# Kernel tuning notes

Measured on AMD Instinct MI355X. Metric: run time of the kernel, lower is better.

Reference implementation:

```python
import jax, jax.numpy as jnp
import numpy as np

N_NODES = 50000
N_EDGES = 800000
IN_DIM = 128
HEADS = 8
HEAD_DIM = 16


def setup_inputs() -> dict:
    key = jax.random.key(0)
    ks = jax.random.split(key, 9)
    s = 1.0 / np.sqrt(IN_DIM)
    return {
        "h": jax.random.normal(ks[0], (N_NODES, IN_DIM), dtype=jnp.float32),
        "src": jax.random.randint(ks[1], (N_EDGES,), 0, N_NODES, dtype=jnp.int32),
        "dst": jax.random.randint(ks[2], (N_EDGES,), 0, N_NODES, dtype=jnp.int32),
        "WQ": jax.random.normal(ks[3], (IN_DIM, HEADS * HEAD_DIM), dtype=jnp.float32) * s,
        "bQ": jnp.zeros((HEADS * HEAD_DIM,), dtype=jnp.float32),
        "WK": jax.random.normal(ks[4], (IN_DIM, HEADS * HEAD_DIM), dtype=jnp.float32) * s,
        "bK": jnp.zeros((HEADS * HEAD_DIM,), dtype=jnp.float32),
        "WV": jax.random.normal(ks[5], (IN_DIM, HEADS * HEAD_DIM), dtype=jnp.float32) * s,
        "bV": jnp.zeros((HEADS * HEAD_DIM,), dtype=jnp.float32),
    }


def reference(h, src, dst, WQ, bQ, WK, bK, WV, bV):
    N = h.shape[0]
    sqrt_d = jnp.float32(np.sqrt(HEAD_DIM))
    # node projections, viewed as [N, H, D]
    Q = (h @ WQ + bQ).reshape(N, HEADS, HEAD_DIM)
    K = (h @ WK + bK).reshape(N, HEADS, HEAD_DIM)
    V = (h @ WV + bV).reshape(N, HEADS, HEAD_DIM)
    # edge scores: (K_src . Q_dst) per head, scaled exp with clamp [-5, 5]
    score = jnp.sum(K[src] * Q[dst], axis=-1, keepdims=True)  # [E, H, 1]
    score = jnp.exp(jnp.clip(score / sqrt_d, -5.0, 5.0))
    # segment-softmax denominator z and weighted V sum wV, both scattered to dst
    z = jax.ops.segment_sum(score, dst, num_segments=N)            # [N, H, 1]
    wV = jax.ops.segment_sum(V[src] * score, dst, num_segments=N)  # [N, H, D]
    # possible_empty: divide only where z > 0 (wV is 0 there anyway)
    head_out = jnp.where(z > 0, wV / jnp.where(z > 0, z, 1.0), wV)
    return head_out
```

## Files before the change

### kernel.cpp

```cpp
#include <hip/hip_runtime.h>
#include <math.h>

#define DIM 128
#define N_HEADS 8
#define HD 16

typedef __attribute__((ext_vector_type(8))) short bf16x8;
typedef __attribute__((ext_vector_type(4))) float f32x4;

__device__ __forceinline__ unsigned bf16pack2(float a, float b) {
    unsigned ua = __builtin_bit_cast(unsigned, a);
    unsigned ub = __builtin_bit_cast(unsigned, b);
    ua = (ua + 0x7FFFu + ((ua >> 16) & 1u)) >> 16;
    ub = (ub + 0x7FFFu + ((ub >> 16) & 1u)) >> 16;
    return ua | (ub << 16);
}
__device__ __forceinline__ float bf16lo(unsigned p) {
    return __builtin_bit_cast(float, p << 16);
}
__device__ __forceinline__ float bf16hi(unsigned p) {
    return __builtin_bit_cast(float, p & 0xFFFF0000u);
}

__global__ __launch_bounds__(256)
void convert_hist_kernel(const float* __restrict__ WQ, const float* __restrict__ bQ,
                         const float* __restrict__ WK, const float* __restrict__ bK,
                         const float* __restrict__ WV, const float* __restrict__ bV,
                         unsigned short* __restrict__ WT, float* __restrict__ bias384,
                         const int* __restrict__ dst, int* __restrict__ offs,
                         int nConv, int E)
{
    if ((int)blockIdx.x < nConv) {
        int idx = blockIdx.x * 256 + threadIdx.x;
        int c = idx >> 7, k = idx & 127;
        const float* W; const float* b; int col = c & 127;
        if (c < 128)      { W = WQ; b = bQ; }
        else if (c < 256) { W = WK; b = bK; }
        else              { W = WV; b = bV; }
        float v = W[k * DIM + col];
        WT[(size_t)c * DIM + k] = (unsigned short)(bf16pack2(v, 0.0f) & 0xFFFFu);
        if (k == 0) bias384[c] = b[col];
    } else {
        int e = ((int)blockIdx.x - nConv) * 256 + threadIdx.x;
        if (e < E) atomicAdd(&offs[dst[e]], 1);
    }
}

__global__ __launch_bounds__(256)
void scan_blocks_kernel(int* __restrict__ offs, int* __restrict__ bsum, int N)
{
    __shared__ int sd[256];
    const int t = threadIdx.x;
    const int i = blockIdx.x * 256 + t;
    int v = (i < N) ? offs[i] : 0;
    sd[t] = v;
    __syncthreads();
    #pragma unroll
    for (int o = 1; o < 256; o <<= 1) {
        int x = (t >= o) ? sd[t - o] : 0;
        __syncthreads();
        sd[t] += x;
        __syncthreads();
    }
    int incl = sd[t];
    if (i < N) offs[i] = incl - v;
    if (t == 255) bsum[blockIdx.x] = incl;
}

__global__ __launch_bounds__(256)
void scan_fixup_kernel(int* __restrict__ offs, int* __restrict__ cursor,
                       const int* __restrict__ bsum, int nb, int N, int E)
{
    __shared__ int sd[256];
    const int t = threadIdx.x;
    sd[t] = (t < nb && t < (int)blockIdx.x) ? bsum[t] : 0;
    __syncthreads();
    #pragma unroll
    for (int o = 128; o > 0; o >>= 1) {
        if (t < o) sd[t] += sd[t + o];
        __syncthreads();
    }
    const int base = sd[0];
    int i = blockIdx.x * 256 + t;
    if (i < N) {
        int v = offs[i] + base;
        offs[i]   = v;
        cursor[i] = v;
    }
    if (i == 0) offs[N] = E;
}

__global__ __launch_bounds__(256)
void qkv_scatter_kernel(const float* __restrict__ h,
                        const unsigned short* __restrict__ WT,
                        const float* __restrict__ bias384,
                        float* __restrict__ Q, unsigned* __restrict__ KVd,
                        const int* __restrict__ src, const int* __restrict__ dst,
                        int* __restrict__ cursor, int* __restrict__ srcs,
                        int nQkv, int N, int E)
{
    __shared__ unsigned short hs[64 * 136];
    const int tid = threadIdx.x;

    if ((int)blockIdx.x >= nQkv) {
        int e = ((int)blockIdx.x - nQkv) * 256 + tid;
        if (e < E) {
            int d   = dst[e];
            int pos = atomicAdd(&cursor[d], 1);
            srcs[pos] = src[e];
        }
        return;
    }

    const int n0 = blockIdx.x * 64;

    #pragma unroll
    for (int i = 0; i < 4; ++i) {
        int lin  = i * 256 + tid;
        int node = lin >> 4;
        int k0   = (lin & 15) * 8;
        int gn   = n0 + node;
        float4 a0, a1;
        if (gn < N) {
            a0 = *(const float4*)(h + (size_t)gn * DIM + k0);
            a1 = *(const float4*)(h + (size_t)gn * DIM + k0 + 4);
        } else {
            a0 = make_float4(0.f, 0.f, 0.f, 0.f);
            a1 = a0;
        }
        uint4 p = make_uint4(bf16pack2(a0.x, a0.y), bf16pack2(a0.z, a0.w),
                             bf16pack2(a1.x, a1.y), bf16pack2(a1.z, a1.w));
        *(uint4*)(hs + node * 136 + k0) = p;
    }
    __syncthreads();

    const int wave   = tid >> 6;
    const int l      = tid & 63;
    const int lane16 = l & 15;
    const int quad   = l >> 4;
    const int wc0    = wave * 96;

    f32x4 acc[4][6];
    #pragma unroll
    for (int ct = 0; ct < 6; ++ct) {
        float bv = bias384[wc0 + ct * 16 + lane16];
        #pragma unroll
        for (int rt = 0; rt < 4; ++rt)
            acc[rt][ct] = (f32x4){bv, bv, bv, bv};
    }

    #pragma unroll
    for (int ks = 0; ks < 4; ++ks) {
        bf16x8 a[4], b[6];
        #pragma unroll
        for (int rt = 0; rt < 4; ++rt)
            a[rt] = *(const bf16x8*)(hs + (rt * 16 + lane16) * 136 + ks * 32 + quad * 8);
        #pragma unroll
        for (int ct = 0; ct < 6; ++ct)
            b[ct] = *(const bf16x8*)(WT + (size_t)(wc0 + ct * 16 + lane16) * DIM
                                         + ks * 32 + quad * 8);
        #pragma unroll
        for (int rt = 0; rt < 4; ++rt)
            #pragma unroll
            for (int ct = 0; ct < 6; ++ct)
                acc[rt][ct] = __builtin_amdgcn_mfma_f32_16x16x32_bf16(
                    a[rt], b[ct], acc[rt][ct], 0, 0, 0);
    }

    const bool evenlane = (lane16 & 1) == 0;
    #pragma unroll
    for (int rt = 0; rt < 4; ++rt) {
        #pragma unroll
        for (int ct = 0; ct < 6; ++ct) {
            int col = wc0 + ct * 16 + lane16;
            #pragma unroll
            for (int i = 0; i < 4; ++i) {
                float v  = acc[rt][ct][i];
                float vn = __shfl_xor(v, 1);
                int gn = n0 + rt * 16 + quad * 4 + i;
                if (evenlane && gn < N) {
                    if (col < 128) {
                        *(float2*)(Q + (size_t)gn * DIM + col) = make_float2(v, vn);
                    } else if (col < 256) {
                        KVd[(size_t)gn * 128 + (col - 128)] = bf16pack2(v, vn);
                    } else {
                        KVd[(size_t)gn * 128 + (col - 256) + 1] = bf16pack2(v, vn);
                    }
                }
            }
        }
    }
}

__device__ __forceinline__ void agg_step(uint2 kv, float2 q,
                                         float& ax, float& ay, float& zs)
{
    float p = bf16lo(kv.x) * q.x + bf16hi(kv.x) * q.y;
    p += __shfl_xor(p, 4);
    p += __shfl_xor(p, 2);
    p += __shfl_xor(p, 1);
    p = fminf(fmaxf(p * 0.25f, -5.0f), 5.0f);
    float w = __expf(p);
    ax += w * bf16lo(kv.y);
    ay += w * bf16hi(kv.y);
    zs += w;
}

__global__ __launch_bounds__(256)
void aggregate_kernel(const int* __restrict__ offs, const int* __restrict__ srcs,
                      const float* __restrict__ Q, const unsigned* __restrict__ KVd,
                      float* __restrict__ out, int N)
{
    const int node = blockIdx.x * 4 + (threadIdx.x >> 6);
    if (node >= N) return;
    const int l = threadIdx.x & 63;

    const float2 q = *(const float2*)(Q + (size_t)node * DIM + 2 * l);
    const int start = offs[node];
    const int end   = offs[node + 1];

    float ax = 0.0f, ay = 0.0f, zs = 0.0f;

    int e = start;
    for (; e + 4 <= end; e += 4) {
        int s0 = srcs[e], s1 = srcs[e + 1], s2 = srcs[e + 2], s3 = srcs[e + 3];
        uint2 kv0 = *(const uint2*)(KVd + (size_t)s0 * 128 + 2 * l);
        uint2 kv1 = *(const uint2*)(KVd + (size_t)s1 * 128 + 2 * l);
        uint2 kv2 = *(const uint2*)(KVd + (size_t)s2 * 128 + 2 * l);
        uint2 kv3 = *(const uint2*)(KVd + (size_t)s3 * 128 + 2 * l);
        float p0 = bf16lo(kv0.x) * q.x + bf16hi(kv0.x) * q.y;
        float p1 = bf16lo(kv1.x) * q.x + bf16hi(kv1.x) * q.y;
        float p2 = bf16lo(kv2.x) * q.x + bf16hi(kv2.x) * q.y;
        float p3 = bf16lo(kv3.x) * q.x + bf16hi(kv3.x) * q.y;
        p0 += __shfl_xor(p0, 4); p1 += __shfl_xor(p1, 4);
        p2 += __shfl_xor(p2, 4); p3 += __shfl_xor(p3, 4);
        p0 += __shfl_xor(p0, 2); p1 += __shfl_xor(p1, 2);
        p2 += __shfl_xor(p2, 2); p3 += __shfl_xor(p3, 2);
        p0 += __shfl_xor(p0, 1); p1 += __shfl_xor(p1, 1);
        p2 += __shfl_xor(p2, 1); p3 += __shfl_xor(p3, 1);
        p0 = fminf(fmaxf(p0 * 0.25f, -5.0f), 5.0f);
        p1 = fminf(fmaxf(p1 * 0.25f, -5.0f), 5.0f);
        p2 = fminf(fmaxf(p2 * 0.25f, -5.0f), 5.0f);
        p3 = fminf(fmaxf(p3 * 0.25f, -5.0f), 5.0f);
        float w0 = __expf(p0), w1 = __expf(p1), w2 = __expf(p2), w3 = __expf(p3);
        ax += w0 * bf16lo(kv0.y); ay += w0 * bf16hi(kv0.y); zs += w0;
        ax += w1 * bf16lo(kv1.y); ay += w1 * bf16hi(kv1.y); zs += w1;
        ax += w2 * bf16lo(kv2.y); ay += w2 * bf16hi(kv2.y); zs += w2;
        ax += w3 * bf16lo(kv3.y); ay += w3 * bf16hi(kv3.y); zs += w3;
    }
    for (; e < end; ++e) {
        int s0 = srcs[e];
        uint2 kv0 = *(const uint2*)(KVd + (size_t)s0 * 128 + 2 * l);
        agg_step(kv0, q, ax, ay, zs);
    }

    float inv = (zs > 0.0f) ? (1.0f / zs) : 0.0f;
    *(float2*)(out + (size_t)node * DIM + 2 * l) = make_float2(ax * inv, ay * inv);
}

extern "C" void kernel_launch(void* const* d_in, const int* in_sizes, int n_in,
                              void* d_out, int out_size, void* d_ws, size_t ws_size,
                              hipStream_t stream) {
    const float* h   = (const float*)d_in[0];
    const int*   src = (const int*)  d_in[1];
    const int*   dst = (const int*)  d_in[2];
    const float* WQ  = (const float*)d_in[3];
    const float* bQ  = (const float*)d_in[4];
    const float* WK  = (const float*)d_in[5];
    const float* bK  = (const float*)d_in[6];
    const float* WV  = (const float*)d_in[7];
    const float* bV  = (const float*)d_in[8];
    float* out = (float*)d_out;

    const int N  = in_sizes[0] / DIM;
    const int E  = in_sizes[1];
    const int NB = (N + 255) / 256;
    const int EB = (E + 255) / 256;
    const int nConv = (384 * DIM) / 256;
    const int nQkv  = (N + 63) / 64;

    char* w = (char*)d_ws;
    float*          Q       = (float*)w;           w += (size_t)N * DIM * sizeof(float);
    unsigned*       KVd     = (unsigned*)w;        w += (size_t)N * 128 * sizeof(unsigned);
    unsigned short* WT      = (unsigned short*)w;  w += (size_t)384 * DIM * sizeof(unsigned short);
    float*          bias384 = (float*)w;           w += 384 * sizeof(float);
    int*            offs    = (int*)w;             w += (size_t)(N + 1) * sizeof(int);
    int*            cursor  = (int*)w;             w += (size_t)N * sizeof(int);
    int*            bsum    = (int*)w;             w += 256 * sizeof(int);
    int*            srcs    = (int*)w;

    hipMemsetAsync(offs, 0, (size_t)(N + 1) * sizeof(int), stream);

    convert_hist_kernel<<<nConv + EB, 256, 0, stream>>>(WQ, bQ, WK, bK, WV, bV,
                                                        WT, bias384, dst, offs,
                                                        nConv, E);
    scan_blocks_kernel<<<NB, 256, 0, stream>>>(offs, bsum, N);
    scan_fixup_kernel<<<NB, 256, 0, stream>>>(offs, cursor, bsum, NB, N, E);
    qkv_scatter_kernel<<<nQkv + EB, 256, 0, stream>>>(h, WT, bias384, Q, KVd,
                                                      src, dst, cursor, srcs,
                                                      nQkv, N, E);
    aggregate_kernel<<<(N + 3) / 4, 256, 0, stream>>>(offs, srcs, Q, KVd, out, N);
}
```

Measured before the change: 265.9 us.

## Split scatter from QKV GEMM, transpose MFMA operands for vector stores, unroll aggregation by eight

The fused QKV+scatter kernel is split into two separate launches. The MFMA operands are swapped (weights as A, nodes as B), so each lane holds four consecutive output columns of one node. Q can then be written as float4 and KV as packed pairs without cross-lane shuffles. The aggregation loop gains an 8-edge unrolled body to keep more gathers in flight, at the cost of one extra launch and higher register pressure.

```diff
diff --git a/kernel.cpp b/kernel.cpp
--- a/kernel.cpp
+++ b/kernel.cpp
@@ -91,28 +91,27 @@
 }
 
 __global__ __launch_bounds__(256)
-void qkv_scatter_kernel(const float* __restrict__ h,
-                        const unsigned short* __restrict__ WT,
-                        const float* __restrict__ bias384,
-                        float* __restrict__ Q, unsigned* __restrict__ KVd,
-                        const int* __restrict__ src, const int* __restrict__ dst,
-                        int* __restrict__ cursor, int* __restrict__ srcs,
-                        int nQkv, int N, int E)
+void scatter_kernel(const int* __restrict__ src, const int* __restrict__ dst,
+                    int* __restrict__ cursor, int* __restrict__ srcs, int E)
+{
+    int e = blockIdx.x * 256 + threadIdx.x;
+    if (e < E) {
+        int d   = dst[e];
+        int pos = atomicAdd(&cursor[d], 1);
+        srcs[pos] = src[e];
+    }
+}
+
+__global__ __launch_bounds__(256)
+void qkv_mfma_kernel(const float* __restrict__ h,
+                     const unsigned short* __restrict__ WT,
+                     const float* __restrict__ bias384,
+                     float* __restrict__ Q, unsigned* __restrict__ KVd,
+                     int N)
 {
     __shared__ unsigned short hs[64 * 136];
     const int tid = threadIdx.x;
-
-    if ((int)blockIdx.x >= nQkv) {
-        int e = ((int)blockIdx.x - nQkv) * 256 + tid;
-        if (e < E) {
-            int d   = dst[e];
-            int pos = atomicAdd(&cursor[d], 1);
-            srcs[pos] = src[e];
-        }
-        return;
-    }
-
-    const int n0 = blockIdx.x * 64;
+    const int n0  = blockIdx.x * 64;
 
     #pragma unroll
     for (int i = 0; i < 4; ++i) {
@@ -140,53 +139,52 @@
     const int quad   = l >> 4;
     const int wc0    = wave * 96;
 
-    f32x4 acc[4][6];
+    f32x4 acc[6][4];
     #pragma unroll
     for (int ct = 0; ct < 6; ++ct) {
-        float bv = bias384[wc0 + ct * 16 + lane16];
+        float4 bv = *(const float4*)(bias384 + wc0 + ct * 16 + quad * 4);
         #pragma unroll
         for (int rt = 0; rt < 4; ++rt)
-            acc[rt][ct] = (f32x4){bv, bv, bv, bv};
+            acc[ct][rt] = (f32x4){bv.x, bv.y, bv.z, bv.w};
     }
 
     #pragma unroll
     for (int ks = 0; ks < 4; ++ks) {
-        bf16x8 a[4], b[6];
+        bf16x8 a[6], b[4];
+        #pragma unroll
+        for (int ct = 0; ct < 6; ++ct)
+            a[ct] = *(const bf16x8*)(WT + (size_t)(wc0 + ct * 16 + lane16) * DIM
+                                         + ks * 32 + quad * 8);
         #pragma unroll
         for (int rt = 0; rt < 4; ++rt)
-            a[rt] = *(const bf16x8*)(hs + (rt * 16 + lane16) * 136 + ks * 32 + quad * 8);
+            b[rt] = *(const bf16x8*)(hs + (rt * 16 + lane16) * 136 + ks * 32 + quad * 8);
         #pragma unroll
         for (int ct = 0; ct < 6; ++ct)
-            b[ct] = *(const bf16x8*)(WT + (size_t)(wc0 + ct * 16 + lane16) * DIM
-                                         + ks * 32 + quad * 8);
-        #pragma unroll
-        for (int rt = 0; rt < 4; ++rt)
             #pragma unroll
-            for (int ct = 0; ct < 6; ++ct)
-                acc[rt][ct] = __builtin_amdgcn_mfma_f32_16x16x32_bf16(
-                    a[rt], b[ct], acc[rt][ct], 0, 0, 0);
-    }
-
-    const bool evenlane = (lane16 & 1) == 0;
-    #pragma unroll
-    for (int rt = 0; rt < 4; ++rt) {
-        #pragma unroll
-        for (int ct = 0; ct < 6; ++ct) {
-            int col = wc0 + ct * 16 + lane16;
-            #pragma unroll
-            for (int i = 0; i < 4; ++i) {
-                float v  = acc[rt][ct][i];
-                float vn = __shfl_xor(v, 1);
-                int gn = n0 + rt * 16 + quad * 4 + i;
-                if (evenlane && gn < N) {
-                    if (col < 128) {
-                        *(float2*)(Q + (size_t)gn * DIM + col) = make_float2(v, vn);
-                    } else if (col < 256) {
-                        KVd[(size_t)gn * 128 + (col - 128)] = bf16pack2(v, vn);
-                    } else {
-                        KVd[(size_t)gn * 128 + (col - 256) + 1] = bf16pack2(v, vn);
-                    }
-                }
+            for (int rt = 0; rt < 4; ++rt)
+                acc[ct][rt] = __builtin_amdgcn_mfma_f32_16x16x32_bf16(
+                    a[ct], b[rt], acc[ct][rt], 0, 0, 0);
+    }
+
+    #pragma unroll
+    for (int ct = 0; ct < 6; ++ct) {
+        const int col = wc0 + ct * 16 + quad * 4;
+        #pragma unroll
+        for (int rt = 0; rt < 4; ++rt) {
+            int gn = n0 + rt * 16 + lane16;
+            if (gn >= N) continue;
+            f32x4 v = acc[ct][rt];
+            if (col < 128) {
+                *(float4*)(Q + (size_t)gn * DIM + col) =
+                    make_float4(v[0], v[1], v[2], v[3]);
+            } else if (col < 256) {
+                int c = col - 128;
+                KVd[(size_t)gn * 128 + c]     = bf16pack2(v[0], v[1]);
+                KVd[(size_t)gn * 128 + c + 2] = bf16pack2(v[2], v[3]);
+            } else {
+                int c = col - 256;
+                KVd[(size_t)gn * 128 + c + 1] = bf16pack2(v[0], v[1]);
+                KVd[(size_t)gn * 128 + c + 3] = bf16pack2(v[2], v[3]);
             }
         }
     }
@@ -222,31 +220,57 @@
     float ax = 0.0f, ay = 0.0f, zs = 0.0f;
 
     int e = start;
+    for (; e + 8 <= end; e += 8) {
+        uint2 kv[8];
+        #pragma unroll
+        for (int j = 0; j < 8; ++j) {
+            int s = srcs[e + j];
+            kv[j] = *(const uint2*)(KVd + (size_t)s * 128 + 2 * l);
+        }
+        float p[8];
+        #pragma unroll
+        for (int j = 0; j < 8; ++j)
+            p[j] = bf16lo(kv[j].x) * q.x + bf16hi(kv[j].x) * q.y;
+        #pragma unroll
+        for (int j = 0; j < 8; ++j) p[j] += __shfl_xor(p[j], 4);
+        #pragma unroll
+        for (int j = 0; j < 8; ++j) p[j] += __shfl_xor(p[j], 2);
+        #pragma unroll
+        for (int j = 0; j < 8; ++j) p[j] += __shfl_xor(p[j], 1);
+        #pragma unroll
+        for (int j = 0; j < 8; ++j) {
+            float pc = fminf(fmaxf(p[j] * 0.25f, -5.0f), 5.0f);
+            float w  = __expf(pc);
+            ax += w * bf16lo(kv[j].y);
+            ay += w * bf16hi(kv[j].y);
+            zs += w;
+        }
+    }
     for (; e + 4 <= end; e += 4) {
-        int s0 = srcs[e], s1 = srcs[e + 1], s2 = srcs[e + 2], s3 = srcs[e + 3];
-        uint2 kv0 = *(const uint2*)(KVd + (size_t)s0 * 128 + 2 * l);
-        uint2 kv1 = *(const uint2*)(KVd + (size_t)s1 * 128 + 2 * l);
-        uint2 kv2 = *(const uint2*)(KVd + (size_t)s2 * 128 + 2 * l);
-        uint2 kv3 = *(const uint2*)(KVd + (size_t)s3 * 128 + 2 * l);
-        float p0 = bf16lo(kv0.x) * q.x + bf16hi(kv0.x) * q.y;
-        float p1 = bf16lo(kv1.x) * q.x + bf16hi(kv1.x) * q.y;
-        float p2 = bf16lo(kv2.x) * q.x + bf16hi(kv2.x) * q.y;
-        float p3 = bf16lo(kv3.x) * q.x + bf16hi(kv3.x) * q.y;
-        p0 += __shfl_xor(p0, 4); p1 += __shfl_xor(p1, 4);
-        p2 += __shfl_xor(p2, 4); p3 += __shfl_xor(p3, 4);
-        p0 += __shfl_xor(p0, 2); p1 += __shfl_xor(p1, 2);
-        p2 += __shfl_xor(p2, 2); p3 += __shfl_xor(p3, 2);
-        p0 += __shfl_xor(p0, 1); p1 += __shfl_xor(p1, 1);
-        p2 += __shfl_xor(p2, 1); p3 += __shfl_xor(p3, 1);
-        p0 = fminf(fmaxf(p0 * 0.25f, -5.0f), 5.0f);
-        p1 = fminf(fmaxf(p1 * 0.25f, -5.0f), 5.0f);
-        p2 = fminf(fmaxf(p2 * 0.25f, -5.0f), 5.0f);
-        p3 = fminf(fmaxf(p3 * 0.25f, -5.0f), 5.0f);
-        float w0 = __expf(p0), w1 = __expf(p1), w2 = __expf(p2), w3 = __expf(p3);
-        ax += w0 * bf16lo(kv0.y); ay += w0 * bf16hi(kv0.y); zs += w0;
-        ax += w1 * bf16lo(kv1.y); ay += w1 * bf16hi(kv1.y); zs += w1;
-        ax += w2 * bf16lo(kv2.y); ay += w2 * bf16hi(kv2.y); zs += w2;
-        ax += w3 * bf16lo(kv3.y); ay += w3 * bf16hi(kv3.y); zs += w3;
+        uint2 kv[4];
+        #pragma unroll
+        for (int j = 0; j < 4; ++j) {
+            int s = srcs[e + j];
+            kv[j] = *(const uint2*)(KVd + (size_t)s * 128 + 2 * l);
+        }
+        float p[4];
+        #pragma unroll
+        for (int j = 0; j < 4; ++j)
+            p[j] = bf16lo(kv[j].x) * q.x + bf16hi(kv[j].x) * q.y;
+        #pragma unroll
+        for (int j = 0; j < 4; ++j) p[j] += __shfl_xor(p[j], 4);
+        #pragma unroll
+        for (int j = 0; j < 4; ++j) p[j] += __shfl_xor(p[j], 2);
+        #pragma unroll
+        for (int j = 0; j < 4; ++j) p[j] += __shfl_xor(p[j], 1);
+        #pragma unroll
+        for (int j = 0; j < 4; ++j) {
+            float pc = fminf(fmaxf(p[j] * 0.25f, -5.0f), 5.0f);
+            float w  = __expf(pc);
+            ax += w * bf16lo(kv[j].y);
+            ay += w * bf16hi(kv[j].y);
+            zs += w;
+        }
     }
     for (; e < end; ++e) {
         int s0 = srcs[e];
@@ -277,7 +301,6 @@
     const int NB = (N + 255) / 256;
     const int EB = (E + 255) / 256;
     const int nConv = (384 * DIM) / 256;
-    const int nQkv  = (N + 63) / 64;
 
     char* w = (char*)d_ws;
     float*          Q       = (float*)w;           w += (size_t)N * DIM * sizeof(float);
@@ -296,8 +319,7 @@
                                                         nConv, E);
     scan_blocks_kernel<<<NB, 256, 0, stream>>>(offs, bsum, N);
     scan_fixup_kernel<<<NB, 256, 0, stream>>>(offs, cursor, bsum, NB, N, E);
-    qkv_scatter_kernel<<<nQkv + EB, 256, 0, stream>>>(h, WT, bias384, Q, KVd,
-                                                      src, dst, cursor, srcs,
-                                                      nQkv, N, E);
+    scatter_kernel<<<EB, 256, 0, stream>>>(src, dst, cursor, srcs, E);
+    qkv_mfma_kernel<<<(N + 63) / 64, 256, 0, stream>>>(h, WT, bias384, Q, KVd, N);
     aggregate_kernel<<<(N + 3) / 4, 256, 0, stream>>>(offs, srcs, Q, KVd, out, N);
 }
```

Measured after the change: 263.4 us. No clear change (-0.9%).
